# Kernel tuning notes

Measured on AMD Instinct MI355X. Metric: run time of the kernel, lower is better.

Reference implementation:

```python
import jax, jax.numpy as jnp
import numpy as np

B, L, E, H = 2, 2048, 1024, 16
D = E // H


def _complex_linear(xr, xi, Wr, Wi, br, bi):
    # (xr + i*xi) @ (Wr + i*Wi)^T + (br + i*bi)
    yr = xr @ Wr.T - xi @ Wi.T + br
    yi = xr @ Wi.T + xi @ Wr.T + bi
    return yr, yi


def _split_heads(x):
    # [B, L, E] -> [B, H, L, D]
    return x.reshape(B, -1, H, D).transpose(0, 2, 1, 3)


def setup_inputs() -> dict:
    key = jax.random.key(0)
    ks = jax.random.split(key, 32)
    s = 1.0 / np.sqrt(E)
    inp = {}
    names = ["query_r", "query_i", "key_r", "key_i", "value_r", "value_i"]
    for i, n in enumerate(names):
        inp[n] = jax.random.normal(ks[i], (B, L, E), dtype=jnp.float32)
    j = 6
    for p in ["q", "k", "v", "o"]:
        inp[f"W{p}_r"] = jax.random.normal(ks[j], (E, E), dtype=jnp.float32) * s; j += 1
        inp[f"W{p}_i"] = jax.random.normal(ks[j], (E, E), dtype=jnp.float32) * s; j += 1
        inp[f"b{p}_r"] = jax.random.normal(ks[j], (E,), dtype=jnp.float32) * 0.01; j += 1
        inp[f"b{p}_i"] = jax.random.normal(ks[j], (E,), dtype=jnp.float32) * 0.01; j += 1
    return inp


def reference(query_r, query_i, key_r, key_i, value_r, value_i,
              Wq_r, Wq_i, bq_r, bq_i,
              Wk_r, Wk_i, bk_r, bk_i,
              Wv_r, Wv_i, bv_r, bv_i,
              Wo_r, Wo_i, bo_r, bo_i):
    qr, qi = _complex_linear(query_r, query_i, Wq_r, Wq_i, bq_r, bq_i)
    kr, ki = _complex_linear(key_r, key_i, Wk_r, Wk_i, bk_r, bk_i)
    vr, vi = _complex_linear(value_r, value_i, Wv_r, Wv_i, bv_r, bv_i)
    qr, qi = _split_heads(qr), _split_heads(qi)
    kr, ki = _split_heads(kr), _split_heads(ki)
    vr, vi = _split_heads(vr), _split_heads(vi)
    scale = jnp.float32(1.0 / np.sqrt(D))
    # Re(q @ conj(k)^T) = qr.kr^T + qi.ki^T  (imag part of scores is discarded)
    scores = (jnp.einsum('bhld,bhmd->bhlm', qr, kr)
              + jnp.einsum('bhld,bhmd->bhlm', qi, ki)) * scale
    probs = jax.nn.softmax(scores, axis=-1)  # real probs
    out_r = jnp.einsum('bhlm,bhmd->bhld', probs, vr)
    out_i = jnp.einsum('bhlm,bhmd->bhld', probs, vi)
    out_r = out_r.transpose(0, 2, 1, 3).reshape(B, L, E)
    out_i = out_i.transpose(0, 2, 1, 3).reshape(B, L, E)
    yr, yi = _complex_linear(out_r, out_i, Wo_r, Wo_i, bo_r, bo_i)
    return jnp.stack([yr, yi])  # [2, B, L, E] = (real, imag)
```

## Files before the change

kernel.cpp:

```cpp
#include <hip/hip_runtime.h>


#define LL 2048
#define EE 1024
#define HH 16
#define BL 4096
#define KK 2048

typedef __attribute__((ext_vector_type(8))) short bf16x8;
typedef __attribute__((ext_vector_type(4))) float f32x4;
typedef unsigned short u16;

__device__ __forceinline__ u16 f2bf(float x) {
    unsigned u = __builtin_bit_cast(unsigned, x);
    u += 0x7fff + ((u >> 16) & 1);
    return (u16)(u >> 16);
}

__device__ __forceinline__ void gl2lds16(const void* g, void* l) {
    __builtin_amdgcn_global_load_lds((const __attribute__((address_space(1))) void*)g,
                                     (__attribute__((address_space(3))) void*)l, 16, 0, 0);
}

struct ConvXArgs { const float* src[6]; u16* dst[6]; };
__global__ void conv_x(ConvXArgs a) {
    const int z = blockIdx.y;
    int i = blockIdx.x * 256 + threadIdx.x;
    float4 v = ((const float4*)a.src[z])[i];
    ushort4 o;
    o.x = f2bf(v.x); o.y = f2bf(v.y); o.z = f2bf(v.z); o.w = f2bf(v.w);
    ((ushort4*)a.dst[z])[i] = o;
}

struct ConvWArgs { const float* wr[4]; const float* wi[4]; u16* w2[4]; };
__global__ void conv_w(ConvWArgs a) {
    const int z = blockIdx.y;
    int i = blockIdx.x * 256 + threadIdx.x;
    int n = i >> 9, k = (i & 511) << 2;
    bool nh = n >= EE, kh = k >= EE;
    int nn = n & (EE - 1), kk = k & (EE - 1);
    const float* src = nh ? (kh ? a.wr[z] : a.wi[z]) : (kh ? a.wi[z] : a.wr[z]);
    float sgn = (!nh && kh) ? -1.0f : 1.0f;
    float4 v = *(const float4*)(src + nn * EE + kk);
    ushort4 o;
    o.x = f2bf(v.x * sgn); o.y = f2bf(v.y * sgn);
    o.z = f2bf(v.z * sgn); o.w = f2bf(v.w * sgn);
    *(ushort4*)(a.w2[z] + n * KK + k) = o;
}

#define GEMM_BK64_LOOP(Ar, Ai, B2)                                             \
    for (int k0 = 0; k0 < KK; k0 += 64) {                                      \
        const u16* Asrc = (k0 < EE) ? (Ar + k0) : (Ai + (k0 - EE));            \
        const u16* Bsrc = B2 + k0;                                             \
        __syncthreads();                                                       \
        {                                                                      \
            int rr = lane >> 3, cg = (lane & 7) ^ rr;                          \
            for (int t = 0; t < 4; t++) {                                      \
                int s = wave * 4 + t;                                          \
                int r0 = s * 8 + rr;                                           \
                gl2lds16(Asrc + (size_t)(m0 + r0) * EE + cg * 8, &As[s * 512]);\
                gl2lds16(Bsrc + (size_t)(n0 + r0) * KK + cg * 8, &Bs[s * 512]);\
            }                                                                  \
        }                                                                      \
        __syncthreads();                                                       \
        for (int ks2 = 0; ks2 < 2; ks2++) {                                    \
            bf16x8 a[4], b[4];                                                 \
            for (int t = 0; t < 4; t++) {                                      \
                int ra = wm + t * 16 + l16;                                    \
                a[t] = *(const bf16x8*)&As[ra * 64 + (((ks2 * 4 + quad) ^ (ra & 7)) << 3)]; \
                int rb = wn + t * 16 + l16;                                    \
                b[t] = *(const bf16x8*)&Bs[rb * 64 + (((ks2 * 4 + quad) ^ (rb & 7)) << 3)]; \
            }                                                                  \
            for (int i = 0; i < 4; i++)                                        \
                for (int j = 0; j < 4; j++)                                    \
                    acc[i][j] = __builtin_amdgcn_mfma_f32_16x16x32_bf16(a[i], b[j], acc[i][j], 0, 0, 0); \
        }                                                                      \
    }

struct QKVArgs {
    const u16* Ar[3]; const u16* Ai[3]; const u16* B2[3];
    const float* br[3]; const float* bi[3];
    u16* out[3];
    float oscale[3];
};

#define BAR      asm volatile("s_barrier" ::: "memory")
#define BARW(N)  asm volatile("s_waitcnt vmcnt(" #N ")\n\ts_barrier" ::: "memory")

#define LOAD_A(QM)                                                             \
    { const u16* base_ = &AB[buf][0][QM][0];                                   \
      _Pragma("unroll") for (int i_ = 0; i_ < 4; i_++) {                       \
          int row_ = wr * 64 + i_ * 16 + l16;                                  \
          _Pragma("unroll") for (int s_ = 0; s_ < 2; s_++) {                   \
              int ph_ = (s_ * 4 + quad) ^ (l16 & 7);                           \
              afr[i_][s_] = *(const bf16x8*)&base_[row_ * 64 + ph_ * 8];       \
          } } }

#define LOAD_B(QN)                                                             \
    { const u16* base_ = &AB[buf][1][QN][0];                                   \
      _Pragma("unroll") for (int j_ = 0; j_ < 2; j_++) {                       \
          int row_ = wc * 32 + j_ * 16 + l16;                                  \
          _Pragma("unroll") for (int s_ = 0; s_ < 2; s_++) {                   \
              int ph_ = (s_ * 4 + quad) ^ (l16 & 7);                           \
              bfr[QN][j_][s_] = *(const bf16x8*)&base_[row_ * 64 + ph_ * 8];   \
          } } }

#define MMA(QM, QN)                                                            \
    { __builtin_amdgcn_s_setprio(1);                                           \
      _Pragma("unroll") for (int s_ = 0; s_ < 2; s_++)                         \
          _Pragma("unroll") for (int i_ = 0; i_ < 4; i_++)                     \
              _Pragma("unroll") for (int j_ = 0; j_ < 2; j_++)                 \
                  acc[QM * 4 + i_][QN * 2 + j_] =                              \
                      __builtin_amdgcn_mfma_f32_16x16x32_bf16(                 \
                          afr[i_][s_], bfr[QN][j_][s_],                        \
                          acc[QM * 4 + i_][QN * 2 + j_], 0, 0, 0);             \
      __builtin_amdgcn_s_setprio(0); }

#define STAGE_A(BUF, HALF, K0)                                                 \
    { const u16* S_ = ((K0) < EE) ? (Apr + (K0)) : (Api + ((K0) - EE));        \
      int rl_ = wv * 8 + (lane >> 3);                                          \
      int cg_ = ((lane & 7) ^ (lane >> 3)) * 8;                                \
      gl2lds16(S_ + (size_t)(m0 + (HALF) * 128 + rl_) * EE + cg_,              \
               &AB[BUF][0][HALF][wv * 512]);                                   \
      gl2lds16(S_ + (size_t)(m0 + (HALF) * 128 + rl_ + 64) * EE + cg_,         \
               &AB[BUF][0][HALF][wv * 512 + 4096]); }

#define STAGE_B(BUF, HALF, K0)                                                 \
    { const u16* S_ = Bp + (K0);                                               \
      int rl_ = wv * 8 + (lane >> 3);                                          \
      int cg_ = ((lane & 7) ^ (lane >> 3)) * 8;                                \
      gl2lds16(S_ + (size_t)(n0 + (HALF) * 128 + rl_) * (size_t)KK + cg_,      \
               &AB[BUF][1][HALF][wv * 512]);                                   \
      gl2lds16(S_ + (size_t)(n0 + (HALF) * 128 + rl_ + 64) * (size_t)KK + cg_, \
               &AB[BUF][1][HALF][wv * 512 + 4096]); }

__launch_bounds__(512, 2)
__global__ void gemm_qkv(QKVArgs args) {
    __shared__ __attribute__((aligned(16))) u16 AB[2][2][2][8192];

    const int z = blockIdx.z;
    const u16* __restrict__ Apr = args.Ar[z];
    const u16* __restrict__ Api = args.Ai[z];
    const u16* __restrict__ Bp  = args.B2[z];

    const int tid = threadIdx.x, wv = tid >> 6, lane = tid & 63;
    const int quad = lane >> 4, l16 = lane & 15;
    const int m0 = blockIdx.y * 256, n0 = blockIdx.x * 256;
    const int wr = wv >> 2, wc = wv & 3;

    f32x4 acc[8][4] = {};
    bf16x8 afr[4][2];
    bf16x8 bfr[2][2][2];

    STAGE_A(0, 0, 0); STAGE_B(0, 0, 0); STAGE_B(0, 1, 0); STAGE_A(0, 1, 0);
    BARW(4);

    for (int T = 0; T < 31; T++) {
        const int buf = T & 1, nb = buf ^ 1;
        const int k1 = T * 64 + 64;
        LOAD_A(0); LOAD_B(0);
        STAGE_A(nb, 0, k1);
        BAR;
        MMA(0, 0);
        BARW(4);
        LOAD_B(1);
        STAGE_B(nb, 0, k1);
        BAR;
        MMA(0, 1);
        BARW(4);
        LOAD_A(1);
        STAGE_B(nb, 1, k1);
        BAR;
        MMA(1, 1);
        BAR;
        STAGE_A(nb, 1, k1);
        BAR;
        MMA(1, 0);
        BARW(4);
    }
    {
        const int buf = 1;
        LOAD_A(0); LOAD_B(0);
        MMA(0, 0);
        BARW(2);
        LOAD_B(1);
        MMA(0, 1);
        BARW(0);
        LOAD_A(1);
        MMA(1, 1);
        MMA(1, 0);
    }

    const float* __restrict__ br_ = args.br[z];
    const float* __restrict__ bi_ = args.bi[z];
    u16* __restrict__ out = args.out[z];
    const float oscale = args.oscale[z];

    #pragma unroll
    for (int j = 0; j < 4; j++) {
        int gn = n0 + (j >> 1) * 128 + wc * 32 + (j & 1) * 16 + l16;
        int ri = gn >> 10, e = gn & 1023;
        float bias = ri ? bi_[e] : br_[e];
        int h = e >> 6, d = e & 63;
        #pragma unroll
        for (int i = 0; i < 8; i++) {
            int gmb = m0 + (i >> 2) * 128 + wr * 64 + (i & 3) * 16 + quad * 4;
            #pragma unroll
            for (int r = 0; r < 4; r++) {
                int gm = gmb + r;
                float v = (acc[i][j][r] + bias) * oscale;
                int b = gm >> 11, l = gm & 2047;
                if (z < 2)
                    out[((size_t)(b * HH + h) * LL + l) * 128 + ri * 64 + d] = f2bf(v);
                else
                    out[((size_t)(b * HH + h) * 128 + ri * 64 + d) * LL + l] = f2bf(v);
            }
        }
    }
}

__launch_bounds__(256, 2)
__global__ void gemm_oproj(const u16* __restrict__ Ar, const u16* __restrict__ Ai,
                           const u16* __restrict__ B2,
                           const float* __restrict__ br, const float* __restrict__ bi,
                           float* __restrict__ out)
{
    __shared__ __attribute__((aligned(16))) u16 As[128 * 64];
    __shared__ __attribute__((aligned(16))) u16 Bs[128 * 64];

    const int tid = threadIdx.x, wave = tid >> 6, lane = tid & 63;
    const int quad = lane >> 4, l16 = lane & 15;
    const int m0 = blockIdx.y * 128, n0 = blockIdx.x * 128;
    const int wm = (wave >> 1) * 64, wn = (wave & 1) * 64;

    f32x4 acc[4][4] = {};

    GEMM_BK64_LOOP(Ar, Ai, B2)

    for (int j = 0; j < 4; j++) {
        int gn = n0 + wn + j * 16 + l16;
        int ri = gn >> 10, e = gn & 1023;
        float bias = ri ? bi[e] : br[e];
        for (int i = 0; i < 4; i++) {
            int gmb = m0 + wm + i * 16 + quad * 4;
            for (int r = 0; r < 4; r++) {
                int gm = gmb + r;
                out[ri * (BL * EE) + gm * EE + e] = acc[i][j][r] + bias;
            }
        }
    }
}

__launch_bounds__(256, 3)
__global__ void attn(const u16* __restrict__ q_ws, const u16* __restrict__ k_ws,
                     const u16* __restrict__ v_ws,
                     u16* __restrict__ o_r, u16* __restrict__ o_i)
{
    __shared__ __attribute__((aligned(16))) u16 kbuf[2][64 * 128];
    __shared__ __attribute__((aligned(16))) u16 vbuf[128 * 64];
    __shared__ __attribute__((aligned(16))) float red_sh[4][16];

    const int tid = threadIdx.x, wave = tid >> 6, lane = tid & 63;
    const int quad = lane >> 4, l16 = lane & 15;
    const int q0 = blockIdx.x * 64, bh = blockIdx.y;

    bf16x8 qf[4];
    {
        const u16* qp = q_ws + (size_t)(bh * LL + q0 + wave * 16 + l16) * 128 + quad * 8;
        for (int ks = 0; ks < 4; ks++)
            qf[ks] = *(const bf16x8*)(qp + ks * 32);
    }

    auto stage_k = [&](int nb, int kv0) {
        for (int t = 0; t < 4; t++) {
            int s = wave * 4 + t;
            int row = s * 4 + (lane >> 4);
            int cg = (lane & 15) ^ (row & 15);
            gl2lds16(k_ws + (size_t)(bh * LL + kv0 + row) * 128 + cg * 8, &kbuf[nb][s * 512]);
        }
    };
    auto stage_v = [&](int kv0) {
        for (int t = 0; t < 4; t++) {
            int s = wave * 4 + t;
            int row = s * 8 + (lane >> 3);
            int cg = (lane & 7) ^ (row & 7);
            gl2lds16(v_ws + (size_t)(bh * 128 + row) * LL + kv0 + cg * 8, &vbuf[s * 512]);
        }
    };

    stage_k(0, 0);
    stage_v(0);
    stage_k(1, 64);
    __syncthreads();

    f32x4 oacc[8] = {};
    float m_st = -__builtin_inff();
    float l_st = 0.f;

    for (int N = 0; N < 32; N++) {
        const int cur = N & 1;
        u16* K = kbuf[cur];

        f32x4 s[4] = {};
        for (int ks = 0; ks < 4; ks++) {
            bf16x8 kf[4];
            for (int mt = 0; mt < 4; mt++) {
                int row = mt * 16 + l16;
                int cl = (ks * 4 + quad) ^ (row & 15);
                kf[mt] = *(const bf16x8*)&K[row * 128 + cl * 8];
            }
            for (int mt = 0; mt < 4; mt++)
                s[mt] = __builtin_amdgcn_mfma_f32_16x16x32_bf16(kf[mt], qf[ks], s[mt], 0, 0, 0);
        }

        bool changed = false;
        float alpha;
        {
            float mx = -__builtin_inff();
            for (int mt = 0; mt < 4; mt++)
                for (int r = 0; r < 4; r++)
                    mx = fmaxf(mx, s[mt][r]);
            mx = fmaxf(mx, __shfl_xor(mx, 16, 64));
            mx = fmaxf(mx, __shfl_xor(mx, 32, 64));
            float mnew = fmaxf(m_st, mx);
            changed = (mnew != m_st);
            alpha = __builtin_amdgcn_exp2f(m_st - mnew);
            m_st = mnew;
            float sum = 0.f;
            for (int mt = 0; mt < 4; mt++)
                for (int r = 0; r < 4; r++) {
                    float p = __builtin_amdgcn_exp2f(s[mt][r] - mnew);
                    s[mt][r] = p;
                    sum += p;
                }
            sum += __shfl_xor(sum, 16, 64);
            sum += __shfl_xor(sum, 32, 64);
            l_st = l_st * alpha + sum;
            if (quad == 0) red_sh[wave][l16] = alpha;
        }
        __syncthreads();

        u16* P = kbuf[cur] + wave * 1024;
        for (int mt = 0; mt < 4; mt++) {
            int q = l16;
            int cg = mt * 2 + (quad >> 1);
            int cl = cg ^ (q & 7);
            ushort4 pk;
            pk.x = f2bf(s[mt][0]); pk.y = f2bf(s[mt][1]);
            pk.z = f2bf(s[mt][2]); pk.w = f2bf(s[mt][3]);
            *(ushort4*)&P[q * 64 + cl * 8 + (quad & 1) * 4] = pk;
        }

        if (__any(changed)) {
            f32x4 av = *(const f32x4*)&red_sh[wave][quad * 4];
            for (int nt = 0; nt < 8; nt++)
                oacc[nt] *= av;
        }

        for (int ks = 0; ks < 2; ks++) {
            int clp = (ks * 4 + quad) ^ (l16 & 7);
            bf16x8 pf = *(const bf16x8*)&P[l16 * 64 + clp * 8];
            for (int nt = 0; nt < 8; nt++) {
                int row = nt * 16 + l16;
                int cl = (ks * 4 + quad) ^ (row & 7);
                bf16x8 vf = *(const bf16x8*)&vbuf[row * 64 + cl * 8];
                oacc[nt] = __builtin_amdgcn_mfma_f32_16x16x32_bf16(pf, vf, oacc[nt], 0, 0, 0);
            }
        }
        __syncthreads();

        if (N + 2 < 32) stage_k(cur, (N + 2) * 64);
        if (N + 1 < 32) stage_v((N + 1) * 64);
    }

    if (quad == 0) red_sh[wave][l16] = l_st;
    __syncthreads();
    f32x4 lv = *(const f32x4*)&red_sh[wave][quad * 4];
    f32x4 inv;
    for (int r = 0; r < 4; r++) inv[r] = 1.0f / lv[r];
    const int b = bh >> 4, h = bh & 15;
    for (int nt = 0; nt < 8; nt++) {
        int d2 = nt * 16 + l16;
        u16* op = (d2 < 64) ? o_r : o_i;
        int col = h * 64 + (d2 & 63);
        for (int r = 0; r < 4; r++) {
            int l = q0 + wave * 16 + quad * 4 + r;
            op[(size_t)(b * LL + l) * EE + col] = f2bf(oacc[nt][r] * inv[r]);
        }
    }
}

extern "C" void kernel_launch(void* const* d_in, const int* in_sizes, int n_in,
                              void* d_out, int out_size, void* d_ws, size_t ws_size,
                              hipStream_t stream) {
    const float* bq_r = (const float*)d_in[8];
    const float* bq_i = (const float*)d_in[9];
    const float* bk_r = (const float*)d_in[12];
    const float* bk_i = (const float*)d_in[13];
    const float* bv_r = (const float*)d_in[16];
    const float* bv_i = (const float*)d_in[17];
    const float* bo_r = (const float*)d_in[20];
    const float* bo_i = (const float*)d_in[21];

    u16* ws = (u16*)d_ws;
    const size_t XN = 4194304;
    u16* xqr = ws;            u16* xqi = xqr + XN;
    u16* xkr = xqi + XN;      u16* xki = xkr + XN;
    u16* xvr = xki + XN;      u16* xvi = xvr + XN;
    u16* w2q = xvi + XN;
    u16* w2k = w2q + XN;
    u16* w2v = w2k + XN;
    u16* w2o = w2v + XN;
    u16* q_ws = w2o + XN;
    u16* k_ws = q_ws + 8388608;
    u16* v_ws = k_ws + 8388608;
    u16* o_r = xqr;
    u16* o_i = xqr + XN;

    dim3 blk(256);

    ConvXArgs cx;
    cx.src[0] = (const float*)d_in[0]; cx.dst[0] = xqr;
    cx.src[1] = (const float*)d_in[1]; cx.dst[1] = xqi;
    cx.src[2] = (const float*)d_in[2]; cx.dst[2] = xkr;
    cx.src[3] = (const float*)d_in[3]; cx.dst[3] = xki;
    cx.src[4] = (const float*)d_in[4]; cx.dst[4] = xvr;
    cx.src[5] = (const float*)d_in[5]; cx.dst[5] = xvi;
    conv_x<<<dim3(4096, 6), blk, 0, stream>>>(cx);

    ConvWArgs cw;
    cw.wr[0] = (const float*)d_in[6];  cw.wi[0] = (const float*)d_in[7];  cw.w2[0] = w2q;
    cw.wr[1] = (const float*)d_in[10]; cw.wi[1] = (const float*)d_in[11]; cw.w2[1] = w2k;
    cw.wr[2] = (const float*)d_in[14]; cw.wi[2] = (const float*)d_in[15]; cw.w2[2] = w2v;
    cw.wr[3] = (const float*)d_in[18]; cw.wi[3] = (const float*)d_in[19]; cw.w2[3] = w2o;
    conv_w<<<dim3(4096, 4), blk, 0, stream>>>(cw);

    const float QSCALE = 0.125f * 1.44269504088896f;
    QKVArgs qa;
    qa.Ar[0] = xqr; qa.Ai[0] = xqi; qa.B2[0] = w2q; qa.br[0] = bq_r; qa.bi[0] = bq_i; qa.out[0] = q_ws; qa.oscale[0] = QSCALE;
    qa.Ar[1] = xkr; qa.Ai[1] = xki; qa.B2[1] = w2k; qa.br[1] = bk_r; qa.bi[1] = bk_i; qa.out[1] = k_ws; qa.oscale[1] = 1.0f;
    qa.Ar[2] = xvr; qa.Ai[2] = xvi; qa.B2[2] = w2v; qa.br[2] = bv_r; qa.bi[2] = bv_i; qa.out[2] = v_ws; qa.oscale[2] = 1.0f;
    gemm_qkv<<<dim3(8, 16, 3), dim3(512), 0, stream>>>(qa);

    attn<<<dim3(32, 32), blk, 0, stream>>>(q_ws, k_ws, v_ws, o_r, o_i);

    gemm_oproj<<<dim3(16, 32), blk, 0, stream>>>(o_r, o_i, w2o, bo_r, bo_i, (float*)d_out);
}
```

Baseline: 492.9 us.

## Prefetch two k-tiles ahead in QKV GEMM and unroll loop by two

Restructures the QKV projection GEMM main loop so global-to-LDS staging runs two K-steps ahead instead of one. Both LDS buffers are filled in the prologue, the loop is unrolled by two, and each half refills its own buffer with the tile two steps ahead. Several barrier waits are dropped or relaxed to vmcnt(8), aiming to hide more global load latency behind MFMA work. The cost is more loads in flight and tighter ordering between LDS reads and overwrites of the same buffer, which is a correctness risk.

```diff
diff --git a/kernel.cpp b/kernel.cpp
--- a/kernel.cpp
+++ b/kernel.cpp
@@ -152,43 +152,57 @@
     bf16x8 afr[4][2];
     bf16x8 bfr[2][2][2];
 
-    STAGE_A(0, 0, 0); STAGE_B(0, 0, 0); STAGE_B(0, 1, 0); STAGE_A(0, 1, 0);
-    BARW(4);
-
-    for (int T = 0; T < 31; T++) {
-        const int buf = T & 1, nb = buf ^ 1;
-        const int k1 = T * 64 + 64;
-        LOAD_A(0); LOAD_B(0);
-        STAGE_A(nb, 0, k1);
-        BAR;
-        MMA(0, 0);
-        BARW(4);
-        LOAD_B(1);
-        STAGE_B(nb, 0, k1);
-        BAR;
-        MMA(0, 1);
-        BARW(4);
-        LOAD_A(1);
-        STAGE_B(nb, 1, k1);
-        BAR;
-        MMA(1, 1);
-        BAR;
-        STAGE_A(nb, 1, k1);
-        BAR;
-        MMA(1, 0);
-        BARW(4);
+    STAGE_A(0, 0, 0);  STAGE_B(0, 0, 0);  STAGE_B(0, 1, 0);  STAGE_A(0, 1, 0);
+    STAGE_A(1, 0, 64); STAGE_B(1, 0, 64); STAGE_B(1, 1, 64); STAGE_A(1, 1, 64);
+    BARW(8);
+
+    for (int T2 = 0; T2 < 15; T2++) {
+        const int ke = (2 * T2 + 2) * 64, ko = (2 * T2 + 3) * 64;
+        {
+            const int buf = 0;
+            LOAD_A(0); LOAD_B(0);
+            BAR;  MMA(0, 0);
+            LOAD_B(1);
+            STAGE_A(0, 0, ke); STAGE_B(0, 0, ke);
+            BAR;  MMA(0, 1);
+            LOAD_A(1);
+            STAGE_B(0, 1, ke);
+            BAR;  MMA(1, 1);
+            STAGE_A(0, 1, ke);
+            BARW(8);
+            MMA(1, 0);
+        }
+        {
+            const int buf = 1;
+            LOAD_A(0); LOAD_B(0);
+            BAR;  MMA(0, 0);
+            LOAD_B(1);
+            STAGE_A(1, 0, ko); STAGE_B(1, 0, ko);
+            BAR;  MMA(0, 1);
+            LOAD_A(1);
+            STAGE_B(1, 1, ko);
+            BAR;  MMA(1, 1);
+            STAGE_A(1, 1, ko);
+            BARW(8);
+            MMA(1, 0);
+        }
     }
     {
-        const int buf = 1;
-        LOAD_A(0); LOAD_B(0);
-        MMA(0, 0);
-        BARW(2);
-        LOAD_B(1);
-        MMA(0, 1);
+        {
+            const int buf = 0;
+            LOAD_A(0); LOAD_B(0); MMA(0, 0);
+            LOAD_B(1);            MMA(0, 1);
+            LOAD_A(1);            MMA(1, 1);
+                                  MMA(1, 0);
+        }
         BARW(0);
-        LOAD_A(1);
-        MMA(1, 1);
-        MMA(1, 0);
+        {
+            const int buf = 1;
+            LOAD_A(0); LOAD_B(0); MMA(0, 0);
+            LOAD_B(1);            MMA(0, 1);
+            LOAD_A(1);            MMA(1, 1);
+                                  MMA(1, 0);
+        }
     }
 
     const float* __restrict__ br_ = args.br[z];
```

Measured after the change: 486.3 us. No clear change (-1.3%).
